# Optimization experiments

Measured on AMD Instinct MI355X. Metric: run time of the kernel, lower is better.

The kernel has to match this reference:

```python
import jax, jax.numpy as jnp
import numpy as np

TAU = 1.0
NUM_CLASSES = 14
LOSS_WEIGHT = 1.0


def setup_inputs() -> dict:
    key = jax.random.key(0)
    k1, k2, k3 = jax.random.split(key, 3)
    B, C, H, W = 8, NUM_CLASSES, 512, 512
    preds_S = jax.random.normal(k1, (B, C, H, W), dtype=jnp.float32)
    preds_T = jax.random.normal(k2, (B, C, H, W), dtype=jnp.float32)
    gt_labels = jax.random.randint(k3, (B, 1, H, W), 0, NUM_CLASSES, dtype=jnp.int32)
    return {"preds_S": preds_S, "preds_T": preds_T, "gt_labels": gt_labels}


def _boundaries(gt):
    # gt: [B, H, W] int. Per-class binary mask for classes 1..NUM_CLASSES-1,
    # boundary = mask XOR binary_erosion(mask) with cross (connectivity-1)
    # structuring element and zero border (scipy/cupy ndimage default).
    classes = jnp.arange(1, NUM_CLASSES, dtype=gt.dtype)  # [K]
    m = gt[:, None, :, :] == classes[None, :, None, None]  # [B, K, H, W] bool
    mp = jnp.pad(m, ((0, 0), (0, 0), (1, 1), (1, 1)))  # zero border
    eroded = (m
              & mp[:, :, :-2, 1:-1]   # up
              & mp[:, :, 2:, 1:-1]    # down
              & mp[:, :, 1:-1, :-2]   # left
              & mp[:, :, 1:-1, 2:])   # right
    return m ^ eroded  # [B, K, H, W] bool


def reference(preds_S, preds_T, gt_labels):
    B, C, H, W = preds_S.shape
    P = H * W
    dt = preds_S.dtype

    boundary = _boundaries(gt_labels[:, 0]).reshape(B, NUM_CLASSES - 1, P)
    bf = boundary.astype(dt)  # [B, K, P]

    # Channel-dim (dim=0 of the [C, HW] view) softmax is per-pixel, so
    # gathering boundary pixels then softmaxing == softmax everywhere + mask.
    log_pS = jax.nn.log_softmax(preds_S / TAU, axis=1).reshape(B, C, P)
    log_pT = jax.nn.log_softmax(preds_T / TAU, axis=1).reshape(B, C, P)
    pT = jnp.exp(log_pT)
    # pointwise KL summed over channels, per pixel: [B, P]
    kl_pix = jnp.sum(pT * (log_pT - log_pS), axis=1)

    n = jnp.sum(bf, axis=-1)                              # [B, K] boundary sizes
    kl_sum = jnp.einsum('bkp,bp->bk', bf, kl_pix)         # [B, K]
    # Original skips when idxs.sum() == 0, i.e. sum of flat boundary indices
    # is zero (no boundary pixels, or sole boundary pixel at index 0).
    idx = jnp.arange(P, dtype=dt)
    idx_sum = jnp.einsum('bkp,p->bk', bf, idx)            # [B, K]
    valid = idx_sum > 0
    # F.kl_div reduction='mean' divides by total elements = C * n
    terms = jnp.where(valid, kl_sum / (C * jnp.maximum(n, 1.0)), 0.0)
    loss = LOSS_WEIGHT * (TAU ** 2) * jnp.sum(terms)
    return loss
```

## Files before the change

kernel.cpp:

```cpp
#include <hip/hip_runtime.h>


#define CC 14
#define KB 13
#define BB 8
#define HH 512
#define WW 512
#define PP (HH * WW)

#define NBINS (BB * KB)

__global__ void zero_ws_kernel(float* __restrict__ ws) {
    int i = threadIdx.x;
    if (i < 2 * NBINS) ws[i] = 0.0f;
}

__global__ __launch_bounds__(256) void boundary_kl_kernel(
        const float* __restrict__ S, const float* __restrict__ T,
        const int* __restrict__ gt, float* __restrict__ ws) {
    const int tid = threadIdx.x;
    const int q   = blockIdx.x * 256 + tid;
    const int b   = q >> 18;
    const int p   = q & (PP - 1);

    __shared__ float s_kl[KB + 1];
    __shared__ float s_n[KB + 1];
    if (tid <= KB) { s_kl[tid] = 0.0f; s_n[tid] = 0.0f; }
    __syncthreads();

    const float* Sb = S + (size_t)b * CC * PP + p;
    const float* Tb = T + (size_t)b * CC * PP + p;
    const int*  gtb = gt + (size_t)b * PP;

    float xs[CC], xt[CC];
#pragma unroll
    for (int c = 0; c < CC; ++c) {
        xs[c] = Sb[(size_t)c * PP];
        xt[c] = Tb[(size_t)c * PP];
    }

    const int k = gtb[p];
    const int h = p >> 9;
    const int w = p & (WW - 1);
    const int gu = (h > 0)      ? gtb[p - WW] : -1;
    const int gd = (h < HH - 1) ? gtb[p + WW] : -1;
    const int gl = (w > 0)      ? gtb[p - 1]  : -1;
    const int gr = (w < WW - 1) ? gtb[p + 1]  : -1;
    const bool eroded = (gu == k) & (gd == k) & (gl == k) & (gr == k);
    const bool contrib = (k >= 1) && !eroded;

    float mS = xs[0], mT = xt[0];
#pragma unroll
    for (int c = 1; c < CC; ++c) { mS = fmaxf(mS, xs[c]); mT = fmaxf(mT, xt[c]); }

    float zS = 0.f, zT = 0.f, A = 0.f;
#pragma unroll
    for (int c = 0; c < CC; ++c) {
        float eS = __expf(xs[c] - mS);
        float eT = __expf(xt[c] - mT);
        zS += eS;
        zT += eT;
        A  += eT * (xt[c] - xs[c]);
    }
    const float kl = A / zT + (mS + __logf(zS)) - (mT + __logf(zT));

    if (contrib) {
        atomicAdd(&s_kl[k], kl);
        atomicAdd(&s_n[k], 1.0f);
    }
    __syncthreads();

    if (tid >= 1 && tid <= KB) {
        atomicAdd(&ws[b * KB + (tid - 1)], s_kl[tid]);
        atomicAdd(&ws[NBINS + b * KB + (tid - 1)], s_n[tid]);
    }
}

__global__ void finalize_kernel(const float* __restrict__ ws,
                                const int* __restrict__ gt,
                                float* __restrict__ out) {
    __shared__ float partial[128];
    const int tid = threadIdx.x;
    float t = 0.0f;
    if (tid < NBINS) {
        const int b = tid / KB;
        const int k = (tid % KB) + 1;
        const float kl = ws[tid];
        const float n  = ws[NBINS + tid];
        const int k0 = gt[(size_t)b * PP];
        const float sub = (k0 == k) ? 1.0f : 0.0f;
        const float npos = n - sub;
        t = (npos > 0.0f) ? (kl / ((float)CC * fmaxf(n, 1.0f))) : 0.0f;
    }
    partial[tid] = t;
    __syncthreads();
    for (int s = 64; s > 0; s >>= 1) {
        if (tid < s) partial[tid] += partial[tid + s];
        __syncthreads();
    }
    if (tid == 0) out[0] = partial[0];
}

extern "C" void kernel_launch(void* const* d_in, const int* in_sizes, int n_in,
                              void* d_out, int out_size, void* d_ws, size_t ws_size,
                              hipStream_t stream) {
    const float* S  = (const float*)d_in[0];
    const float* T  = (const float*)d_in[1];
    const int*   gt = (const int*)d_in[2];
    float* out = (float*)d_out;
    float* ws  = (float*)d_ws;

    hipLaunchKernelGGL(zero_ws_kernel, dim3(1), dim3(256), 0, stream, ws);
    hipLaunchKernelGGL(boundary_kl_kernel, dim3(BB * PP / 256), dim3(256), 0, stream,
                       S, T, gt, ws);
    hipLaunchKernelGGL(finalize_kernel, dim3(1), dim3(128), 0, stream, ws, gt, out);
}
```

Baseline: 267.2 us.

## Stage logits tile into LDS via 16-byte global_load_lds DMA

Each block now stages its 256-pixel tile of all 14 student and 14 teacher channels into shared memory using the direct global-to-LDS load builtin with 16-byte lanes. Each wave issues 7 of the 28 channel-chunk loads. The boundary-label neighbour checks run while those loads are in flight, and the per-pixel values are then read back from LDS. The aim is wider, fewer memory transactions and better latency hiding than 28 scalar 4-byte loads per thread. The cost is 28 KB of LDS per block, which may limit occupancy, and the code relies on the compiler inserting the correct wait before the barrier.

```diff
diff --git a/kernel.cpp b/kernel.cpp
--- a/kernel.cpp
+++ b/kernel.cpp
@@ -7,6 +7,9 @@
 #define HH 512
 #define WW 512
 #define PP (HH * WW)
+#define TILE 256
+#define TILES_PER_IMG (PP / TILE)
+#define CHUNKS (2 * CC)
 
 #define NBINS (BB * KB)
 
@@ -18,27 +21,33 @@
 __global__ __launch_bounds__(256) void boundary_kl_kernel(
         const float* __restrict__ S, const float* __restrict__ T,
         const int* __restrict__ gt, float* __restrict__ ws) {
-    const int tid = threadIdx.x;
-    const int q   = blockIdx.x * 256 + tid;
-    const int b   = q >> 18;
-    const int p   = q & (PP - 1);
+    const int tid  = threadIdx.x;
+    const int wid  = tid >> 6;
+    const int lane = tid & 63;
+    const int b    = blockIdx.x / TILES_PER_IMG;
+    const int p0   = (blockIdx.x % TILES_PER_IMG) * TILE;
 
+    __shared__ float lds[CHUNKS * TILE];
     __shared__ float s_kl[KB + 1];
     __shared__ float s_n[KB + 1];
     if (tid <= KB) { s_kl[tid] = 0.0f; s_n[tid] = 0.0f; }
-    __syncthreads();
 
-    const float* Sb = S + (size_t)b * CC * PP + p;
-    const float* Tb = T + (size_t)b * CC * PP + p;
+    const float* Sb = S + (size_t)b * CC * PP + p0;
+    const float* Tb = T + (size_t)b * CC * PP + p0;
     const int*  gtb = gt + (size_t)b * PP;
 
-    float xs[CC], xt[CC];
 #pragma unroll
-    for (int c = 0; c < CC; ++c) {
-        xs[c] = Sb[(size_t)c * PP];
-        xt[c] = Tb[(size_t)c * PP];
+    for (int i = 0; i < 7; ++i) {
+        const int j  = wid * 7 + i;
+        const int ch = (j < CC) ? j : j - CC;
+        const float* gsrc = ((j < CC) ? Sb : Tb) + (size_t)ch * PP + lane * 4;
+        __builtin_amdgcn_global_load_lds(
+            (const __attribute__((address_space(1))) void*)gsrc,
+            (__attribute__((address_space(3))) void*)&lds[j * TILE],
+            16, 0, 0);
     }
 
+    const int p = p0 + tid;
     const int k = gtb[p];
     const int h = p >> 9;
     const int w = p & (WW - 1);
@@ -48,6 +57,15 @@
     const int gr = (w < WW - 1) ? gtb[p + 1]  : -1;
     const bool eroded = (gu == k) & (gd == k) & (gl == k) & (gr == k);
     const bool contrib = (k >= 1) && !eroded;
+
+    __syncthreads();
+
+    float xs[CC], xt[CC];
+#pragma unroll
+    for (int c = 0; c < CC; ++c) {
+        xs[c] = lds[c * TILE + tid];
+        xt[c] = lds[(CC + c) * TILE + tid];
+    }
 
     float mS = xs[0], mT = xt[0];
 #pragma unroll
@@ -111,7 +129,7 @@
     float* ws  = (float*)d_ws;
 
     hipLaunchKernelGGL(zero_ws_kernel, dim3(1), dim3(256), 0, stream, ws);
-    hipLaunchKernelGGL(boundary_kl_kernel, dim3(BB * PP / 256), dim3(256), 0, stream,
+    hipLaunchKernelGGL(boundary_kl_kernel, dim3(BB * TILES_PER_IMG), dim3(256), 0, stream,
                        S, T, gt, ws);
     hipLaunchKernelGGL(finalize_kernel, dim3(1), dim3(128), 0, stream, ws, gt, out);
 }
```

Result: no change. 269.9 us (+1.0%).

## Stage S/T loads through LDS via global_load_lds with multi-tile waves

Applied to the files above, without the earlier changes.

Each wave now processes four 64-pixel tiles in sequence. For each tile it issues direct global-to-LDS loads for all 28 channel values, then computes the boundary mask while those loads are in flight and reads the channels back from LDS. This lowers register pressure and cuts the grid by four, which amortises the per-block shared-atomic flush. The loop is not software-pipelined across tiles, so each tile's loads fully stall before compute, and in-flight memory parallelism per wave may drop.

```diff
diff --git a/kernel.cpp b/kernel.cpp
--- a/kernel.cpp
+++ b/kernel.cpp
@@ -7,6 +7,11 @@
 #define HH 512
 #define WW 512
 #define PP (HH * WW)
+#define TPW 4
+#define TILE 64
+#define PX_PER_BLOCK (4 * TPW * TILE)
+#define BLOCKS_PER_IMG (PP / PX_PER_BLOCK)
+#define WSTRIP (2 * CC * TILE)
 
 #define NBINS (BB * KB)
 
@@ -18,58 +23,84 @@
 __global__ __launch_bounds__(256) void boundary_kl_kernel(
         const float* __restrict__ S, const float* __restrict__ T,
         const int* __restrict__ gt, float* __restrict__ ws) {
-    const int tid = threadIdx.x;
-    const int q   = blockIdx.x * 256 + tid;
-    const int b   = q >> 18;
-    const int p   = q & (PP - 1);
+    const int tid  = threadIdx.x;
+    const int wid  = tid >> 6;
+    const int lane = tid & 63;
+    const int b    = blockIdx.x / BLOCKS_PER_IMG;
+    const int pblk = (blockIdx.x % BLOCKS_PER_IMG) * PX_PER_BLOCK;
 
+    __shared__ float lds[4 * WSTRIP];
     __shared__ float s_kl[KB + 1];
     __shared__ float s_n[KB + 1];
     if (tid <= KB) { s_kl[tid] = 0.0f; s_n[tid] = 0.0f; }
     __syncthreads();
 
-    const float* Sb = S + (size_t)b * CC * PP + p;
-    const float* Tb = T + (size_t)b * CC * PP + p;
+    float* wbuf = &lds[wid * WSTRIP];
+    const float* Sb = S + (size_t)b * CC * PP;
+    const float* Tb = T + (size_t)b * CC * PP;
     const int*  gtb = gt + (size_t)b * PP;
 
-    float xs[CC], xt[CC];
+    for (int t = 0; t < TPW; ++t) {
+        const int p0 = pblk + wid * (TPW * TILE) + t * TILE;
+
 #pragma unroll
-    for (int c = 0; c < CC; ++c) {
-        xs[c] = Sb[(size_t)c * PP];
-        xt[c] = Tb[(size_t)c * PP];
+        for (int c = 0; c < CC; ++c) {
+            __builtin_amdgcn_global_load_lds(
+                (const __attribute__((address_space(1))) void*)(Sb + (size_t)c * PP + p0 + lane),
+                (__attribute__((address_space(3))) void*)&wbuf[c * TILE],
+                4, 0, 0);
+        }
+#pragma unroll
+        for (int c = 0; c < CC; ++c) {
+            __builtin_amdgcn_global_load_lds(
+                (const __attribute__((address_space(1))) void*)(Tb + (size_t)c * PP + p0 + lane),
+                (__attribute__((address_space(3))) void*)&wbuf[(CC + c) * TILE],
+                4, 0, 0);
+        }
+
+        const int p = p0 + lane;
+        const int k = gtb[p];
+        const int h = p >> 9;
+        const int w = p & (WW - 1);
+        const int gu = (h > 0)      ? gtb[p - WW] : -1;
+        const int gd = (h < HH - 1) ? gtb[p + WW] : -1;
+        const int gl = (w > 0)      ? gtb[p - 1]  : -1;
+        const int gr = (w < WW - 1) ? gtb[p + 1]  : -1;
+        const bool eroded = (gu == k) & (gd == k) & (gl == k) & (gr == k);
+        const bool contrib = (k >= 1) && !eroded;
+
+        __builtin_amdgcn_s_waitcnt(0x0F70);
+        __builtin_amdgcn_sched_barrier(0);
+
+        float xs[CC], xt[CC];
+#pragma unroll
+        for (int c = 0; c < CC; ++c) {
+            xs[c] = wbuf[c * TILE + lane];
+            xt[c] = wbuf[(CC + c) * TILE + lane];
+        }
+
+        float mS = xs[0], mT = xt[0];
+#pragma unroll
+        for (int c = 1; c < CC; ++c) { mS = fmaxf(mS, xs[c]); mT = fmaxf(mT, xt[c]); }
+
+        float zS = 0.f, zT = 0.f, A = 0.f;
+#pragma unroll
+        for (int c = 0; c < CC; ++c) {
+            float eS = __expf(xs[c] - mS);
+            float eT = __expf(xt[c] - mT);
+            zS += eS;
+            zT += eT;
+            A  += eT * (xt[c] - xs[c]);
+        }
+        const float kl = A / zT + (mS + __logf(zS)) - (mT + __logf(zT));
+
+        if (contrib) {
+            atomicAdd(&s_kl[k], kl);
+            atomicAdd(&s_n[k], 1.0f);
+        }
     }
 
-    const int k = gtb[p];
-    const int h = p >> 9;
-    const int w = p & (WW - 1);
-    const int gu = (h > 0)      ? gtb[p - WW] : -1;
-    const int gd = (h < HH - 1) ? gtb[p + WW] : -1;
-    const int gl = (w > 0)      ? gtb[p - 1]  : -1;
-    const int gr = (w < WW - 1) ? gtb[p + 1]  : -1;
-    const bool eroded = (gu == k) & (gd == k) & (gl == k) & (gr == k);
-    const bool contrib = (k >= 1) && !eroded;
-
-    float mS = xs[0], mT = xt[0];
-#pragma unroll
-    for (int c = 1; c < CC; ++c) { mS = fmaxf(mS, xs[c]); mT = fmaxf(mT, xt[c]); }
-
-    float zS = 0.f, zT = 0.f, A = 0.f;
-#pragma unroll
-    for (int c = 0; c < CC; ++c) {
-        float eS = __expf(xs[c] - mS);
-        float eT = __expf(xt[c] - mT);
-        zS += eS;
-        zT += eT;
-        A  += eT * (xt[c] - xs[c]);
-    }
-    const float kl = A / zT + (mS + __logf(zS)) - (mT + __logf(zT));
-
-    if (contrib) {
-        atomicAdd(&s_kl[k], kl);
-        atomicAdd(&s_n[k], 1.0f);
-    }
     __syncthreads();
-
     if (tid >= 1 && tid <= KB) {
         atomicAdd(&ws[b * KB + (tid - 1)], s_kl[tid]);
         atomicAdd(&ws[NBINS + b * KB + (tid - 1)], s_n[tid]);
@@ -111,7 +142,7 @@
     float* ws  = (float*)d_ws;
 
     hipLaunchKernelGGL(zero_ws_kernel, dim3(1), dim3(256), 0, stream, ws);
-    hipLaunchKernelGGL(boundary_kl_kernel, dim3(BB * PP / 256), dim3(256), 0, stream,
+    hipLaunchKernelGGL(boundary_kl_kernel, dim3(BB * BLOCKS_PER_IMG), dim3(256), 0, stream,
                        S, T, gt, ws);
     hipLaunchKernelGGL(finalize_kernel, dim3(1), dim3(128), 0, stream, ws, gt, out);
 }
```

After: 257.0 us. 1.04x faster.
